# Kernel optimization log

Hardware: AMD Instinct MI355X
Metric: run time of the kernel (lower is better)

Reference implementation:

```python
import jax, jax.numpy as jnp
import numpy as np

LOG_ZERO = -40.0
LOG_EPS = 1e-10

@jax.custom_vjp
def grad_scale(x):
    return x

def _gs_fwd(x):
    return x, None

def _gs_bwd(_, g):
    return (g * 0.01,)

grad_scale.defvjp(_gs_fwd, _gs_bwd)

def to_log_space(x):
    sign_x = jnp.sign(x)
    sign_x = jnp.where(sign_x == 0, jnp.ones_like(sign_x), sign_x)
    abs_x = jnp.abs(x)
    log_x = jnp.where(abs_x > LOG_EPS, jnp.log(jnp.maximum(abs_x, LOG_EPS)), LOG_ZERO)
    return log_x, sign_x

def from_log_space(log_x, sign_x):
    mask = log_x > LOG_ZERO + 1.0
    res = sign_x * jnp.exp(jnp.minimum(grad_scale(log_x), 20.0))
    return jnp.where(mask, res, jnp.zeros_like(res))

def signed_log_add(log_a, sign_a, log_b, sign_b):
    a_is_zero = log_a <= LOG_ZERO + 1.0
    b_is_zero = log_b <= LOG_ZERO + 1.0
    max_log = jnp.maximum(log_a, log_b)
    min_log = jnp.minimum(log_a, log_b)
    diff = min_log - max_log
    a_is_max = log_a >= log_b
    sign_max = jnp.where(a_is_max, sign_a, sign_b)
    sign_min = jnp.where(a_is_max, sign_b, sign_a)
    same_sign = sign_max * sign_min > 0
    exp_diff = jnp.exp(diff)
    log_same = max_log + jnp.log1p(exp_diff)
    log_opp = max_log + jnp.log1p(-jnp.minimum(exp_diff, 0.9999))
    log_result = jnp.where(same_sign, log_same, log_opp)
    sign_result = sign_max
    log_result = jnp.where(a_is_zero, log_b, log_result)
    sign_result = jnp.where(a_is_zero, sign_b, sign_result)
    log_result = jnp.where(b_is_zero & ~a_is_zero, log_a, log_result)
    sign_result = jnp.where(b_is_zero & ~a_is_zero, sign_a, sign_result)
    return log_result, sign_result

def soft_bound_log(log_h):
    return -jax.nn.softplus(-log_h)


def setup_inputs() -> dict:
    key = jax.random.key(0)
    T, B, D = 512, 16, 1024
    k = jax.random.split(key, 4)
    xav = float(np.sqrt(6.0 / (D + D)))  # xavier_uniform bound base
    return {
        'x': jax.random.normal(k[0], (T, B, D), jnp.float32),
        'W_x': jax.random.uniform(k[1], (D, D), jnp.float32, -0.5 * xav, 0.5 * xav),
        'W_alpha': jax.random.uniform(k[2], (D, D), jnp.float32, -0.1 * xav, 0.1 * xav),
        'W_delta': jax.random.uniform(k[3], (D, D), jnp.float32, -0.1 * xav, 0.1 * xav),
        'b': jnp.zeros(D, jnp.float32),
        'b_alpha': jnp.zeros(D, jnp.float32),
        'b_delta': jnp.full((D,), -2.0, jnp.float32),
        'log_r_h': jnp.full((D,), -2.0, jnp.float32),
        'sign_r_h': jnp.ones(D, jnp.float32),
    }


def reference(x, W_x, W_alpha, W_delta, b, b_alpha, b_delta, log_r_h, sign_r_h):
    T, B, D = x.shape
    # Precompute all input projections (the compute-heavy GEMMs) in one shot.
    alpha_raw = jnp.einsum('tbd,ed->tbe', x, W_alpha) + b_alpha        # [T,B,D]
    alpha = 1.0 + jax.nn.softplus(alpha_raw)
    lin = jnp.einsum('tbd,ed->tbe', x, W_x) + b                        # [T,B,D]
    log_input, sign_input = to_log_space(lin)
    delta_raw = jnp.einsum('tbd,ed->tbe', x, W_delta) + b_delta        # [T,B,D]
    log_delta = jax.nn.log_sigmoid(delta_raw)
    log_1m_delta = jax.nn.log_sigmoid(-delta_raw)

    log_h0 = jnp.full((B, D), LOG_ZERO, x.dtype)
    sign_h0 = jnp.ones((B, D), x.dtype)

    def step(carry, inp):
        log_hp, sign_hp = carry
        a_t, log_in, sign_in, log_d, log_1md = inp
        log_rh = log_r_h + log_hp
        sign_rh = sign_r_h * sign_hp
        log_v, sign_v = signed_log_add(log_rh, sign_rh, log_in, sign_in)
        log_cand = soft_bound_log(a_t * log_v)
        log_h_new, sign_h_new = signed_log_add(log_1md + log_hp, sign_hp,
                                               log_d + log_cand, sign_v)
        h_lin = from_log_space(log_h_new, sign_h_new)
        return (log_h_new, sign_h_new), (log_h_new, sign_h_new, h_lin)

    _, (log_hs, sign_hs, h_linear) = jax.lax.scan(
        step, (log_h0, sign_h0), (alpha, log_input, sign_input, log_delta, log_1m_delta))
    log_h = jnp.concatenate([log_h0[None], log_hs], axis=0)    # [T+1,B,D]
    sign_h = jnp.concatenate([sign_h0[None], sign_hs], axis=0) # [T+1,B,D]
    return log_h, sign_h, h_linear
```

## Files before the change

### kernel.cpp

```cpp
#include <hip/hip_runtime.h>
#include <math.h>

#define BD 16384
#define TT 512
#define KDIM 1024
#define NDIM 1024
#define GEMM_M 8192
#define PANEL_Q 320
#define LOGE2F 0.69314718246459960938f

__device__ __forceinline__ float np_expf(float x)   { return expf(x); }
__device__ __forceinline__ float np_logf(float x)   { return logf(x); }
__device__ __forceinline__ float np_log1pf(float x) { return log1pf(x); }

__device__ __forceinline__ float np_softplus(float v) {
    const float e  = np_expf(-fabsf(v));
    const float l1 = np_log1pf(e);
    const float r  = __fadd_rn(fmaxf(v, 0.0f), l1);
    return (v == 0.0f) ? LOGE2F : r;
}

__device__ __forceinline__ void np_sla(float la, float sa, float lb, float sb,
                                       float& lo, float& so) {
    bool az = la <= -39.0f;
    bool bz = lb <= -39.0f;
    float mx = fmaxf(la, lb);
    float mn = fminf(la, lb);
    float diff = __fsub_rn(mn, mx);
    bool amax = la >= lb;
    float smax = amax ? sa : sb;
    float smin = amax ? sb : sa;
    bool same = __fmul_rn(smax, smin) > 0.0f;
    float ed = np_expf(diff);
    float ls  = __fadd_rn(mx, np_log1pf(ed));
    float lop = __fadd_rn(mx, np_log1pf(-fminf(ed, 0.9999f)));
    float l = same ? ls : lop;
    float s = smax;
    l = az ? lb : l;  s = az ? sb : s;
    bool bo = bz && !az;
    l = bo ? la : l;  s = bo ? sa : s;
    lo = l; so = s;
}

__global__ __launch_bounds__(256) void gemm_blas(
    const float* __restrict__ x,
    const float* __restrict__ Wa, const float* __restrict__ Wx, const float* __restrict__ Wd,
    const float* __restrict__ ba, const float* __restrict__ bx, const float* __restrict__ bd,
    float* __restrict__ out_a, float* __restrict__ out_x, float* __restrict__ out_d)
{
    const int z = blockIdx.z;
    const float* W    = (z == 0) ? Wa : (z == 1) ? Wx : Wd;
    const float* bias = (z == 0) ? ba : (z == 1) ? bx : bd;
    float* out        = (z == 0) ? out_a : (z == 1) ? out_x : out_d;

    const int m0 = blockIdx.x * 64;
    const int n0 = blockIdx.y * 64;

    __shared__ float As[16][68];
    __shared__ float Bs[16][68];

    const int tid = threadIdx.x;
    const int lr = tid >> 2;
    const int lc = tid & 3;
    const int ty = tid >> 4;
    const int tx = tid & 15;

    const float* Ap = x + (size_t)(m0 + lr) * KDIM + lc * 4;
    const float* Bp = W + (size_t)(n0 + lr) * KDIM + lc * 4;

    float4 fa = *(const float4*)Ap;
    float4 fb = *(const float4*)Bp;

    float tot[4][4];
    float acc[4][4];
    #pragma unroll
    for (int i = 0; i < 4; ++i)
        #pragma unroll
        for (int j = 0; j < 4; ++j) { tot[i][j] = 0.0f; acc[i][j] = 0.0f; }

    for (int kt = 0; kt < KDIM; kt += 16) {
        if (kt == PANEL_Q || kt == 2 * PANEL_Q || kt == 3 * PANEL_Q) {
            #pragma unroll
            for (int i = 0; i < 4; ++i)
                #pragma unroll
                for (int j = 0; j < 4; ++j) {
                    tot[i][j] = __fadd_rn(tot[i][j], acc[i][j]);
                    acc[i][j] = 0.0f;
                }
        }
        __syncthreads();
        {
            const float* pa = (const float*)&fa;
            const float* pb = (const float*)&fb;
            #pragma unroll
            for (int c = 0; c < 4; ++c) {
                As[lc * 4 + c][lr] = pa[c];
                Bs[lc * 4 + c][lr] = pb[c];
            }
        }
        __syncthreads();
        if (kt + 16 < KDIM) {
            fa = *(const float4*)(Ap + kt + 16);
            fb = *(const float4*)(Bp + kt + 16);
        }
        #pragma unroll
        for (int kk = 0; kk < 16; ++kk) {
            const float4 a = *(const float4*)&As[kk][ty * 4];
            const float4 b = *(const float4*)&Bs[kk][tx * 4];
            const float av[4] = {a.x, a.y, a.z, a.w};
            const float bv[4] = {b.x, b.y, b.z, b.w};
            #pragma unroll
            for (int i = 0; i < 4; ++i)
                #pragma unroll
                for (int j = 0; j < 4; ++j)
                    acc[i][j] = __fmaf_rn(av[i], bv[j], acc[i][j]);
        }
    }
    #pragma unroll
    for (int i = 0; i < 4; ++i)
        #pragma unroll
        for (int j = 0; j < 4; ++j)
            tot[i][j] = __fadd_rn(tot[i][j], acc[i][j]);

    float bj[4];
    #pragma unroll
    for (int j = 0; j < 4; ++j) bj[j] = bias[n0 + tx * 4 + j];

    #pragma unroll
    for (int i = 0; i < 4; ++i) {
        float4 v;
        float* op = out + (size_t)(m0 + ty * 4 + i) * NDIM + n0 + tx * 4;
        v.x = __fadd_rn(tot[i][0], bj[0]);
        v.y = __fadd_rn(tot[i][1], bj[1]);
        v.z = __fadd_rn(tot[i][2], bj[2]);
        v.w = __fadd_rn(tot[i][3], bj[3]);
        *(float4*)op = v;
    }
}

__device__ __forceinline__ void gl_lds(const float* g, float* l) {
    __builtin_amdgcn_global_load_lds(
        (const __attribute__((address_space(1))) void*)g,
        (__attribute__((address_space(3))) void*)l, 4, 0, 0);
}

#define WAITVM(N) do {                                                   \
    asm volatile("s_waitcnt vmcnt(" #N ")" ::: "memory");                \
    __builtin_amdgcn_sched_barrier(0); } while (0)

__global__ __launch_bounds__(192, 1) void scan_kernel(
    float* __restrict__ log_h, float* __restrict__ sign_h, float* __restrict__ h_lin,
    const float* __restrict__ log_r_h, const float* __restrict__ sign_r_h)
{
    __shared__ float Xr[4][5][4][64];
    __shared__ float Or[4][2][4][64];
    __shared__ float Rr[4][12][64];

    const int wv = threadIdx.x >> 6;
    const int ln = threadIdx.x & 63;
    const int idx = blockIdx.x * 64 + ln;

#define ISSUE_LOADS(GG, SL) do {                                         \
    const int _b = (GG) * 4;                                             \
    _Pragma("unroll")                                                    \
    for (int u = 0; u < 4; ++u) {                                        \
        gl_lds(h_lin  + (size_t)(_b + u) * BD + idx,     &Rr[SL][u * 3 + 0][0]); \
        gl_lds(log_h  + (size_t)(_b + u + 1) * BD + idx, &Rr[SL][u * 3 + 1][0]); \
        gl_lds(sign_h + (size_t)(_b + u + 1) * BD + idx, &Rr[SL][u * 3 + 2][0]); \
    } } while (0)

#define XFORM_TO(GG) do {                                                \
    const int _s = (GG) & 3;                                             \
    _Pragma("unroll")                                                    \
    for (int u = 0; u < 4; ++u) {                                        \
        const float araw = Rr[_s][u * 3 + 0][ln];                        \
        const float lin  = Rr[_s][u * 3 + 1][ln];                        \
        const float dr   = Rr[_s][u * 3 + 2][ln];                        \
        Xr[_s][0][u][ln] = __fadd_rn(1.0f, np_softplus(araw));           \
        const float ax = fabsf(lin);                                     \
        Xr[_s][1][u][ln] = (ax > 1e-10f) ? np_logf(fmaxf(ax, 1e-10f))    \
                                         : -40.0f;                       \
        Xr[_s][2][u][ln] = (lin < 0.0f) ? -1.0f : 1.0f;                  \
        const float e  = np_expf(-fabsf(dr));                            \
        const float l1 = np_log1pf(e);                                   \
        const float big = -__fadd_rn(fabsf(dr), l1);                     \
        const float sml = -l1;                                           \
        const float ld0 = (dr > 0.0f) ? sml : big;                       \
        const float lm0 = (dr > 0.0f) ? big : sml;                       \
        Xr[_s][3][u][ln] = (dr == 0.0f) ? -LOGE2F : ld0;                 \
        Xr[_s][4][u][ln] = (dr == 0.0f) ? -LOGE2F : lm0;                 \
    } } while (0)

#define WRITE_GROUP(GG) do {                                             \
    const int _s = (GG) & 3;                                             \
    _Pragma("unroll")                                                    \
    for (int u = 0; u < 4; ++u) {                                        \
        const int t = (GG) * 4 + u;                                      \
        const float lhn = Or[_s][0][u][ln];                              \
        const float shn = Or[_s][1][u][ln];                              \
        const float res = __fmul_rn(shn, np_expf(fminf(lhn, 20.0f)));    \
        const float h = (lhn > -39.0f) ? res : 0.0f;                     \
        log_h[(size_t)(t + 1) * BD + idx] = lhn;                         \
        sign_h[(size_t)(t + 1) * BD + idx] = shn;                        \
        h_lin[(size_t)t * BD + idx] = h;                                 \
    } } while (0)

    float lrh = 0.0f, srh = 0.0f;
    if (wv == 1) {
        const int d = idx & 1023;
        lrh = log_r_h[d];
        srh = sign_r_h[d];
    } else if (wv == 0) {
        ISSUE_LOADS(0, 0);
        ISSUE_LOADS(1, 1);
        WAITVM(0);
        XFORM_TO(0);
        XFORM_TO(1);
        ISSUE_LOADS(2, 2);
    } else {
        log_h[idx] = -40.0f;
        sign_h[idx] = 1.0f;
    }
    __syncthreads();

    float lhp = -40.0f, shp = 1.0f;

    for (int g = 0; g < 128; ++g) {
        if (wv == 0) {
            const int gl = (g + 3 < 128) ? g + 3 : 127;
            ISSUE_LOADS(gl, (g + 3) & 3);
            WAITVM(12);
            if (g + 2 < 128) XFORM_TO(g + 2);
        } else if (wv == 1) {
            const int s = g & 3;
            float xa[4], xli[4], xsi[4], xld[4], xlm[4];
            #pragma unroll
            for (int u = 0; u < 4; ++u) {
                xa[u]  = Xr[s][0][u][ln];
                xli[u] = Xr[s][1][u][ln];
                xsi[u] = Xr[s][2][u][ln];
                xld[u] = Xr[s][3][u][ln];
                xlm[u] = Xr[s][4][u][ln];
            }
            #pragma unroll
            for (int u = 0; u < 4; ++u) {
                const float log_rh  = __fadd_rn(lrh, lhp);
                const float sign_rh = __fmul_rn(srh, shp);
                float lv, sv;
                np_sla(log_rh, sign_rh, xli[u], xsi[u], lv, sv);
                const float tt = __fmul_rn(xa[u], lv);
                const float log_cand = -np_softplus(-tt);
                float lhn, shn;
                np_sla(__fadd_rn(xlm[u], lhp), shp,
                       __fadd_rn(xld[u], log_cand), sv, lhn, shn);
                Or[s][0][u][ln] = lhn;
                Or[s][1][u][ln] = shn;
                lhp = lhn; shp = shn;
            }
        } else {
            if (g > 0) WRITE_GROUP(g - 1);
        }
        __syncthreads();
    }
    if (wv == 2) WRITE_GROUP(127);

#undef ISSUE_LOADS
#undef XFORM_TO
#undef WRITE_GROUP
}

extern "C" void kernel_launch(void* const* d_in, const int* in_sizes, int n_in,
                              void* d_out, int out_size, void* d_ws, size_t ws_size,
                              hipStream_t stream) {
    const float* x        = (const float*)d_in[0];
    const float* W_x      = (const float*)d_in[1];
    const float* W_alpha  = (const float*)d_in[2];
    const float* W_delta  = (const float*)d_in[3];
    const float* b        = (const float*)d_in[4];
    const float* b_alpha  = (const float*)d_in[5];
    const float* b_delta  = (const float*)d_in[6];
    const float* log_r_h  = (const float*)d_in[7];
    const float* sign_r_h = (const float*)d_in[8];

    float* out    = (float*)d_out;
    float* log_h  = out;
    float* sign_h = out + (size_t)513 * BD;
    float* h_lin  = out + (size_t)2 * 513 * BD;

    dim3 ggrid(GEMM_M / 64, NDIM / 64, 3);
    gemm_blas<<<ggrid, dim3(256), 0, stream>>>(
        x, W_alpha, W_x, W_delta, b_alpha, b, b_delta,
        h_lin, log_h + BD, sign_h + BD);

    scan_kernel<<<dim3(BD / 64), dim3(192), 0, stream>>>(
        log_h, sign_h, h_lin, log_r_h, sign_r_h);
}
```

Before: 1.329 ms.

## Fuse GEMM and scan into one persistent kernel with per-slab readiness flags

Merges the three projection GEMMs and the sequential scan into one launch. 256 blocks loop over GEMM tiles in time-slab order and signal per-slab completion counters, while 256 scan blocks spin on those counters so the scan can start before the whole GEMM finishes. The cost targeted is the serialization between the GEMM and the scan. In exchange the GEMM loses its float4 stores and uses agent-scope scalar atomic stores, the scan's async global-to-LDS loads become synchronous atomic loads, and correctness depends on all scan blocks and GEMM blocks being co-resident, otherwise a deadlock is broken only by the spin guard.

```diff
diff --git a/kernel.cpp b/kernel.cpp
--- a/kernel.cpp
+++ b/kernel.cpp
@@ -8,6 +8,9 @@
 #define GEMM_M 8192
 #define PANEL_Q 320
 #define LOGE2F 0.69314718246459960938f
+#define NGEMM 256
+#define NTILE 6144
+#define AGT __HIP_MEMORY_SCOPE_AGENT
 
 __device__ __forceinline__ float np_expf(float x)   { return expf(x); }
 __device__ __forceinline__ float np_logf(float x)   { return logf(x); }
@@ -42,153 +45,154 @@
     lo = l; so = s;
 }
 
-__global__ __launch_bounds__(256) void gemm_blas(
+__device__ __forceinline__ float ld_agent(const float* p) {
+    return __hip_atomic_load(p, __ATOMIC_RELAXED, AGT);
+}
+__device__ __forceinline__ void st_agent(float* p, float v) {
+    __hip_atomic_store(p, v, __ATOMIC_RELAXED, AGT);
+}
+
+__global__ __launch_bounds__(256, 2) void fused(
     const float* __restrict__ x,
     const float* __restrict__ Wa, const float* __restrict__ Wx, const float* __restrict__ Wd,
     const float* __restrict__ ba, const float* __restrict__ bx, const float* __restrict__ bd,
-    float* __restrict__ out_a, float* __restrict__ out_x, float* __restrict__ out_d)
+    const float* __restrict__ log_r_h, const float* __restrict__ sign_r_h,
+    float* __restrict__ log_h, float* __restrict__ sign_h, float* __restrict__ h_lin,
+    int* __restrict__ done)
 {
-    const int z = blockIdx.z;
-    const float* W    = (z == 0) ? Wa : (z == 1) ? Wx : Wd;
-    const float* bias = (z == 0) ? ba : (z == 1) ? bx : bd;
-    float* out        = (z == 0) ? out_a : (z == 1) ? out_x : out_d;
-
-    const int m0 = blockIdx.x * 64;
-    const int n0 = blockIdx.y * 64;
-
-    __shared__ float As[16][68];
-    __shared__ float Bs[16][68];
-
-    const int tid = threadIdx.x;
-    const int lr = tid >> 2;
-    const int lc = tid & 3;
-    const int ty = tid >> 4;
-    const int tx = tid & 15;
-
-    const float* Ap = x + (size_t)(m0 + lr) * KDIM + lc * 4;
-    const float* Bp = W + (size_t)(n0 + lr) * KDIM + lc * 4;
-
-    float4 fa = *(const float4*)Ap;
-    float4 fb = *(const float4*)Bp;
-
-    float tot[4][4];
-    float acc[4][4];
-    #pragma unroll
-    for (int i = 0; i < 4; ++i)
-        #pragma unroll
-        for (int j = 0; j < 4; ++j) { tot[i][j] = 0.0f; acc[i][j] = 0.0f; }
-
-    for (int kt = 0; kt < KDIM; kt += 16) {
-        if (kt == PANEL_Q || kt == 2 * PANEL_Q || kt == 3 * PANEL_Q) {
+    union SMem {
+        struct { float As[16][68]; float Bs[16][68]; } g;
+        struct { float Xr[4][5][4][64]; float Or[4][2][4][64]; } s;
+    };
+    __shared__ SMem sm;
+
+    if (blockIdx.x < NGEMM) {
+        const int tid = threadIdx.x;
+        const int lr = tid >> 2;
+        const int lc = tid & 3;
+        const int ty = tid >> 4;
+        const int tx = tid & 15;
+
+        for (int T = blockIdx.x; T < NTILE; T += NGEMM) {
+            const int m0i = T / 48;
+            const int rem = T % 48;
+            const int z   = rem >> 4;
+            const int n0  = (rem & 15) * 64;
+            const int m0  = m0i * 64;
+            const float* W    = (z == 0) ? Wa : (z == 1) ? Wx : Wd;
+            const float* bias = (z == 0) ? ba : (z == 1) ? bx : bd;
+            float* out = (z == 0) ? h_lin : (z == 1) ? (log_h + BD) : (sign_h + BD);
+
+            const float* Ap = x + (size_t)(m0 + lr) * KDIM + lc * 4;
+            const float* Bp = W + (size_t)(n0 + lr) * KDIM + lc * 4;
+
+            float4 fa = *(const float4*)Ap;
+            float4 fb = *(const float4*)Bp;
+
+            float tot[4][4], acc[4][4];
             #pragma unroll
             for (int i = 0; i < 4; ++i)
                 #pragma unroll
-                for (int j = 0; j < 4; ++j) {
+                for (int j = 0; j < 4; ++j) { tot[i][j] = 0.0f; acc[i][j] = 0.0f; }
+
+            for (int kt = 0; kt < KDIM; kt += 16) {
+                if (kt == PANEL_Q || kt == 2 * PANEL_Q || kt == 3 * PANEL_Q) {
+                    #pragma unroll
+                    for (int i = 0; i < 4; ++i)
+                        #pragma unroll
+                        for (int j = 0; j < 4; ++j) {
+                            tot[i][j] = __fadd_rn(tot[i][j], acc[i][j]);
+                            acc[i][j] = 0.0f;
+                        }
+                }
+                __syncthreads();
+                {
+                    const float* pa = (const float*)&fa;
+                    const float* pb = (const float*)&fb;
+                    #pragma unroll
+                    for (int c = 0; c < 4; ++c) {
+                        sm.g.As[lc * 4 + c][lr] = pa[c];
+                        sm.g.Bs[lc * 4 + c][lr] = pb[c];
+                    }
+                }
+                __syncthreads();
+                if (kt + 16 < KDIM) {
+                    fa = *(const float4*)(Ap + kt + 16);
+                    fb = *(const float4*)(Bp + kt + 16);
+                }
+                #pragma unroll
+                for (int kk = 0; kk < 16; ++kk) {
+                    const float4 a = *(const float4*)&sm.g.As[kk][ty * 4];
+                    const float4 b = *(const float4*)&sm.g.Bs[kk][tx * 4];
+                    const float av[4] = {a.x, a.y, a.z, a.w};
+                    const float bv[4] = {b.x, b.y, b.z, b.w};
+                    #pragma unroll
+                    for (int i = 0; i < 4; ++i)
+                        #pragma unroll
+                        for (int j = 0; j < 4; ++j)
+                            acc[i][j] = __fmaf_rn(av[i], bv[j], acc[i][j]);
+                }
+            }
+            #pragma unroll
+            for (int i = 0; i < 4; ++i)
+                #pragma unroll
+                for (int j = 0; j < 4; ++j)
                     tot[i][j] = __fadd_rn(tot[i][j], acc[i][j]);
-                    acc[i][j] = 0.0f;
-                }
+
+            float bj[4];
+            #pragma unroll
+            for (int j = 0; j < 4; ++j) bj[j] = bias[n0 + tx * 4 + j];
+
+            #pragma unroll
+            for (int i = 0; i < 4; ++i) {
+                float* op = out + (size_t)(m0 + ty * 4 + i) * NDIM + n0 + tx * 4;
+                #pragma unroll
+                for (int j = 0; j < 4; ++j)
+                    st_agent(op + j, __fadd_rn(tot[i][j], bj[j]));
+            }
+            __syncthreads();
+            if (tid == 0)
+                __hip_atomic_fetch_add(&done[m0i], 1, __ATOMIC_RELEASE, AGT);
         }
-        __syncthreads();
-        {
-            const float* pa = (const float*)&fa;
-            const float* pb = (const float*)&fb;
-            #pragma unroll
-            for (int c = 0; c < 4; ++c) {
-                As[lc * 4 + c][lr] = pa[c];
-                Bs[lc * 4 + c][lr] = pb[c];
-            }
-        }
-        __syncthreads();
-        if (kt + 16 < KDIM) {
-            fa = *(const float4*)(Ap + kt + 16);
-            fb = *(const float4*)(Bp + kt + 16);
-        }
-        #pragma unroll
-        for (int kk = 0; kk < 16; ++kk) {
-            const float4 a = *(const float4*)&As[kk][ty * 4];
-            const float4 b = *(const float4*)&Bs[kk][tx * 4];
-            const float av[4] = {a.x, a.y, a.z, a.w};
-            const float bv[4] = {b.x, b.y, b.z, b.w};
-            #pragma unroll
-            for (int i = 0; i < 4; ++i)
-                #pragma unroll
-                for (int j = 0; j < 4; ++j)
-                    acc[i][j] = __fmaf_rn(av[i], bv[j], acc[i][j]);
-        }
-    }
-    #pragma unroll
-    for (int i = 0; i < 4; ++i)
-        #pragma unroll
-        for (int j = 0; j < 4; ++j)
-            tot[i][j] = __fadd_rn(tot[i][j], acc[i][j]);
-
-    float bj[4];
-    #pragma unroll
-    for (int j = 0; j < 4; ++j) bj[j] = bias[n0 + tx * 4 + j];
-
-    #pragma unroll
-    for (int i = 0; i < 4; ++i) {
-        float4 v;
-        float* op = out + (size_t)(m0 + ty * 4 + i) * NDIM + n0 + tx * 4;
-        v.x = __fadd_rn(tot[i][0], bj[0]);
-        v.y = __fadd_rn(tot[i][1], bj[1]);
-        v.z = __fadd_rn(tot[i][2], bj[2]);
-        v.w = __fadd_rn(tot[i][3], bj[3]);
-        *(float4*)op = v;
-    }
-}
-
-__device__ __forceinline__ void gl_lds(const float* g, float* l) {
-    __builtin_amdgcn_global_load_lds(
-        (const __attribute__((address_space(1))) void*)g,
-        (__attribute__((address_space(3))) void*)l, 4, 0, 0);
-}
-
-#define WAITVM(N) do {                                                   \
-    asm volatile("s_waitcnt vmcnt(" #N ")" ::: "memory");                \
-    __builtin_amdgcn_sched_barrier(0); } while (0)
-
-__global__ __launch_bounds__(192, 1) void scan_kernel(
-    float* __restrict__ log_h, float* __restrict__ sign_h, float* __restrict__ h_lin,
-    const float* __restrict__ log_r_h, const float* __restrict__ sign_r_h)
-{
-    __shared__ float Xr[4][5][4][64];
-    __shared__ float Or[4][2][4][64];
-    __shared__ float Rr[4][12][64];
-
-    const int wv = threadIdx.x >> 6;
-    const int ln = threadIdx.x & 63;
-    const int idx = blockIdx.x * 64 + ln;
-
-#define ISSUE_LOADS(GG, SL) do {                                         \
+    } else {
+        const int sb = blockIdx.x - NGEMM;
+        const int wv = threadIdx.x >> 6;
+        const int ln = threadIdx.x & 63;
+        const int idx = sb * 64 + ln;
+
+#define WAIT_SLAB(S) do {                                                \
+    int _guard = 0;                                                      \
+    while (__hip_atomic_load(&done[S], __ATOMIC_ACQUIRE, AGT) < 48) {    \
+        __builtin_amdgcn_s_sleep(2);                                     \
+        if (++_guard > (1 << 27)) break;    \
+    } } while (0)
+
+#define LOAD_XFORM(GG) do {                                              \
+    const int _s = (GG) & 3;                                             \
     const int _b = (GG) * 4;                                             \
+    float ra[4], rl[4], rd[4];                                           \
     _Pragma("unroll")                                                    \
     for (int u = 0; u < 4; ++u) {                                        \
-        gl_lds(h_lin  + (size_t)(_b + u) * BD + idx,     &Rr[SL][u * 3 + 0][0]); \
-        gl_lds(log_h  + (size_t)(_b + u + 1) * BD + idx, &Rr[SL][u * 3 + 1][0]); \
-        gl_lds(sign_h + (size_t)(_b + u + 1) * BD + idx, &Rr[SL][u * 3 + 2][0]); \
-    } } while (0)
-
-#define XFORM_TO(GG) do {                                                \
-    const int _s = (GG) & 3;                                             \
+        ra[u] = ld_agent(h_lin  + (size_t)(_b + u) * BD + idx);          \
+        rl[u] = ld_agent(log_h  + (size_t)(_b + u + 1) * BD + idx);      \
+        rd[u] = ld_agent(sign_h + (size_t)(_b + u + 1) * BD + idx);      \
+    }                                                                    \
     _Pragma("unroll")                                                    \
     for (int u = 0; u < 4; ++u) {                                        \
-        const float araw = Rr[_s][u * 3 + 0][ln];                        \
-        const float lin  = Rr[_s][u * 3 + 1][ln];                        \
-        const float dr   = Rr[_s][u * 3 + 2][ln];                        \
-        Xr[_s][0][u][ln] = __fadd_rn(1.0f, np_softplus(araw));           \
-        const float ax = fabsf(lin);                                     \
-        Xr[_s][1][u][ln] = (ax > 1e-10f) ? np_logf(fmaxf(ax, 1e-10f))    \
-                                         : -40.0f;                       \
-        Xr[_s][2][u][ln] = (lin < 0.0f) ? -1.0f : 1.0f;                  \
+        sm.s.Xr[_s][0][u][ln] = __fadd_rn(1.0f, np_softplus(ra[u]));     \
+        const float ax = fabsf(rl[u]);                                   \
+        sm.s.Xr[_s][1][u][ln] = (ax > 1e-10f) ? np_logf(fmaxf(ax, 1e-10f)) \
+                                              : -40.0f;                  \
+        sm.s.Xr[_s][2][u][ln] = (rl[u] < 0.0f) ? -1.0f : 1.0f;           \
+        const float dr = rd[u];                                          \
         const float e  = np_expf(-fabsf(dr));                            \
         const float l1 = np_log1pf(e);                                   \
         const float big = -__fadd_rn(fabsf(dr), l1);                     \
         const float sml = -l1;                                           \
         const float ld0 = (dr > 0.0f) ? sml : big;                       \
         const float lm0 = (dr > 0.0f) ? big : sml;                       \
-        Xr[_s][3][u][ln] = (dr == 0.0f) ? -LOGE2F : ld0;                 \
-        Xr[_s][4][u][ln] = (dr == 0.0f) ? -LOGE2F : lm0;                 \
+        sm.s.Xr[_s][3][u][ln] = (dr == 0.0f) ? -LOGE2F : ld0;            \
+        sm.s.Xr[_s][4][u][ln] = (dr == 0.0f) ? -LOGE2F : lm0;            \
     } } while (0)
 
 #define WRITE_GROUP(GG) do {                                             \
@@ -196,8 +200,8 @@
     _Pragma("unroll")                                                    \
     for (int u = 0; u < 4; ++u) {                                        \
         const int t = (GG) * 4 + u;                                      \
-        const float lhn = Or[_s][0][u][ln];                              \
-        const float shn = Or[_s][1][u][ln];                              \
+        const float lhn = sm.s.Or[_s][0][u][ln];                         \
+        const float shn = sm.s.Or[_s][1][u][ln];                         \
         const float res = __fmul_rn(shn, np_expf(fminf(lhn, 20.0f)));    \
         const float h = (lhn > -39.0f) ? res : 0.0f;                     \
         log_h[(size_t)(t + 1) * BD + idx] = lhn;                         \
@@ -205,68 +209,67 @@
         h_lin[(size_t)t * BD + idx] = h;                                 \
     } } while (0)
 
-    float lrh = 0.0f, srh = 0.0f;
-    if (wv == 1) {
-        const int d = idx & 1023;
-        lrh = log_r_h[d];
-        srh = sign_r_h[d];
-    } else if (wv == 0) {
-        ISSUE_LOADS(0, 0);
-        ISSUE_LOADS(1, 1);
-        WAITVM(0);
-        XFORM_TO(0);
-        XFORM_TO(1);
-        ISSUE_LOADS(2, 2);
-    } else {
-        log_h[idx] = -40.0f;
-        sign_h[idx] = 1.0f;
-    }
-    __syncthreads();
-
-    float lhp = -40.0f, shp = 1.0f;
-
-    for (int g = 0; g < 128; ++g) {
+        float lrh = 0.0f, srh = 0.0f;
         if (wv == 0) {
-            const int gl = (g + 3 < 128) ? g + 3 : 127;
-            ISSUE_LOADS(gl, (g + 3) & 3);
-            WAITVM(12);
-            if (g + 2 < 128) XFORM_TO(g + 2);
+            WAIT_SLAB(0);
+            LOAD_XFORM(0);
+            WAIT_SLAB(1);
+            LOAD_XFORM(1);
         } else if (wv == 1) {
-            const int s = g & 3;
-            float xa[4], xli[4], xsi[4], xld[4], xlm[4];
-            #pragma unroll
-            for (int u = 0; u < 4; ++u) {
-                xa[u]  = Xr[s][0][u][ln];
-                xli[u] = Xr[s][1][u][ln];
-                xsi[u] = Xr[s][2][u][ln];
-                xld[u] = Xr[s][3][u][ln];
-                xlm[u] = Xr[s][4][u][ln];
-            }
-            #pragma unroll
-            for (int u = 0; u < 4; ++u) {
-                const float log_rh  = __fadd_rn(lrh, lhp);
-                const float sign_rh = __fmul_rn(srh, shp);
-                float lv, sv;
-                np_sla(log_rh, sign_rh, xli[u], xsi[u], lv, sv);
-                const float tt = __fmul_rn(xa[u], lv);
-                const float log_cand = -np_softplus(-tt);
-                float lhn, shn;
-                np_sla(__fadd_rn(xlm[u], lhp), shp,
-                       __fadd_rn(xld[u], log_cand), sv, lhn, shn);
-                Or[s][0][u][ln] = lhn;
-                Or[s][1][u][ln] = shn;
-                lhp = lhn; shp = shn;
-            }
-        } else {
-            if (g > 0) WRITE_GROUP(g - 1);
+            const int d = idx & 1023;
+            lrh = log_r_h[d];
+            srh = sign_r_h[d];
+        } else if (wv == 2) {
+            log_h[idx] = -40.0f;
+            sign_h[idx] = 1.0f;
         }
         __syncthreads();
+
+        float lhp = -40.0f, shp = 1.0f;
+
+        for (int g = 0; g < 128; ++g) {
+            if (wv == 0) {
+                if (g + 2 < 128) {
+                    WAIT_SLAB(g + 2);
+                    LOAD_XFORM(g + 2);
+                }
+            } else if (wv == 1) {
+                const int s = g & 3;
+                float xa[4], xli[4], xsi[4], xld[4], xlm[4];
+                #pragma unroll
+                for (int u = 0; u < 4; ++u) {
+                    xa[u]  = sm.s.Xr[s][0][u][ln];
+                    xli[u] = sm.s.Xr[s][1][u][ln];
+                    xsi[u] = sm.s.Xr[s][2][u][ln];
+                    xld[u] = sm.s.Xr[s][3][u][ln];
+                    xlm[u] = sm.s.Xr[s][4][u][ln];
+                }
+                #pragma unroll
+                for (int u = 0; u < 4; ++u) {
+                    const float log_rh  = __fadd_rn(lrh, lhp);
+                    const float sign_rh = __fmul_rn(srh, shp);
+                    float lv, sv;
+                    np_sla(log_rh, sign_rh, xli[u], xsi[u], lv, sv);
+                    const float tt = __fmul_rn(xa[u], lv);
+                    const float log_cand = -np_softplus(-tt);
+                    float lhn, shn;
+                    np_sla(__fadd_rn(xlm[u], lhp), shp,
+                           __fadd_rn(xld[u], log_cand), sv, lhn, shn);
+                    sm.s.Or[s][0][u][ln] = lhn;
+                    sm.s.Or[s][1][u][ln] = shn;
+                    lhp = lhn; shp = shn;
+                }
+            } else if (wv == 2) {
+                if (g > 0) WRITE_GROUP(g - 1);
+            }
+            __syncthreads();
+        }
+        if (wv == 2) WRITE_GROUP(127);
+
+#undef WAIT_SLAB
+#undef LOAD_XFORM
+#undef WRITE_GROUP
     }
-    if (wv == 2) WRITE_GROUP(127);
-
-#undef ISSUE_LOADS
-#undef XFORM_TO
-#undef WRITE_GROUP
 }
 
 extern "C" void kernel_launch(void* const* d_in, const int* in_sizes, int n_in,
@@ -287,11 +290,10 @@
     float* sign_h = out + (size_t)513 * BD;
     float* h_lin  = out + (size_t)2 * 513 * BD;
 
-    dim3 ggrid(GEMM_M / 64, NDIM / 64, 3);
-    gemm_blas<<<ggrid, dim3(256), 0, stream>>>(
+    int* done = (int*)d_ws;
+    hipMemsetAsync(done, 0, 128 * sizeof(int), stream);
+
+    fused<<<dim3(NGEMM + 256), dim3(256), 0, stream>>>(
         x, W_alpha, W_x, W_delta, b_alpha, b, b_delta,
-        h_lin, log_h + BD, sign_h + BD);
-
-    scan_kernel<<<dim3(BD / 64), dim3(192), 0, stream>>>(
-        log_h, sign_h, h_lin, log_r_h, sign_r_h);
-}
+        log_r_h, sign_r_h, log_h, sign_h, h_lin, done);
+}
```

Result: slower. 3.193 ms (+140.2%).

## Enlarge GEMM block tile to 128x128 with 8x8 per-thread microtile

Applied to the files above, without the earlier changes.

Grows the fp32 GEMM block tile from 64x64 to 128x128, with each thread computing an 8x8 output block instead of 4x4. This raises arithmetic intensity per shared-memory load and halves global traffic per output, aiming to make the SIMT GEMM less bound by LDS and memory bandwidth. The cost is many more registers (128 accumulators plus the partial-sum totals), which lowers occupancy and risks spills, and a grid of only 1536 blocks.

```diff
diff --git a/kernel.cpp b/kernel.cpp
--- a/kernel.cpp
+++ b/kernel.cpp
@@ -53,11 +53,11 @@
     const float* bias = (z == 0) ? ba : (z == 1) ? bx : bd;
     float* out        = (z == 0) ? out_a : (z == 1) ? out_x : out_d;
 
-    const int m0 = blockIdx.x * 64;
-    const int n0 = blockIdx.y * 64;
-
-    __shared__ float As[16][68];
-    __shared__ float Bs[16][68];
+    const int m0 = blockIdx.x * 128;
+    const int n0 = blockIdx.y * 128;
+
+    __shared__ float As[16][132];
+    __shared__ float Bs[16][132];
 
     const int tid = threadIdx.x;
     const int lr = tid >> 2;
@@ -68,73 +68,84 @@
     const float* Ap = x + (size_t)(m0 + lr) * KDIM + lc * 4;
     const float* Bp = W + (size_t)(n0 + lr) * KDIM + lc * 4;
 
-    float4 fa = *(const float4*)Ap;
-    float4 fb = *(const float4*)Bp;
-
-    float tot[4][4];
-    float acc[4][4];
+    float4 aR0 = *(const float4*)(Ap);
+    float4 aR1 = *(const float4*)(Ap + (size_t)64 * KDIM);
+    float4 bR0 = *(const float4*)(Bp);
+    float4 bR1 = *(const float4*)(Bp + (size_t)64 * KDIM);
+
+    float tot[8][8];
+    float acc[8][8];
     #pragma unroll
-    for (int i = 0; i < 4; ++i)
+    for (int i = 0; i < 8; ++i)
         #pragma unroll
-        for (int j = 0; j < 4; ++j) { tot[i][j] = 0.0f; acc[i][j] = 0.0f; }
+        for (int j = 0; j < 8; ++j) { tot[i][j] = 0.0f; acc[i][j] = 0.0f; }
 
     for (int kt = 0; kt < KDIM; kt += 16) {
         if (kt == PANEL_Q || kt == 2 * PANEL_Q || kt == 3 * PANEL_Q) {
             #pragma unroll
-            for (int i = 0; i < 4; ++i)
+            for (int i = 0; i < 8; ++i)
                 #pragma unroll
-                for (int j = 0; j < 4; ++j) {
+                for (int j = 0; j < 8; ++j) {
                     tot[i][j] = __fadd_rn(tot[i][j], acc[i][j]);
                     acc[i][j] = 0.0f;
                 }
         }
         __syncthreads();
         {
-            const float* pa = (const float*)&fa;
-            const float* pb = (const float*)&fb;
+            const float* a0 = (const float*)&aR0;
+            const float* a1 = (const float*)&aR1;
+            const float* b0 = (const float*)&bR0;
+            const float* b1 = (const float*)&bR1;
             #pragma unroll
             for (int c = 0; c < 4; ++c) {
-                As[lc * 4 + c][lr] = pa[c];
-                Bs[lc * 4 + c][lr] = pb[c];
+                As[lc * 4 + c][lr]      = a0[c];
+                As[lc * 4 + c][lr + 64] = a1[c];
+                Bs[lc * 4 + c][lr]      = b0[c];
+                Bs[lc * 4 + c][lr + 64] = b1[c];
             }
         }
         __syncthreads();
         if (kt + 16 < KDIM) {
-            fa = *(const float4*)(Ap + kt + 16);
-            fb = *(const float4*)(Bp + kt + 16);
+            aR0 = *(const float4*)(Ap + kt + 16);
+            aR1 = *(const float4*)(Ap + (size_t)64 * KDIM + kt + 16);
+            bR0 = *(const float4*)(Bp + kt + 16);
+            bR1 = *(const float4*)(Bp + (size_t)64 * KDIM + kt + 16);
         }
         #pragma unroll
         for (int kk = 0; kk < 16; ++kk) {
-            const float4 a = *(const float4*)&As[kk][ty * 4];
-            const float4 b = *(const float4*)&Bs[kk][tx * 4];
-            const float av[4] = {a.x, a.y, a.z, a.w};
-            const float bv[4] = {b.x, b.y, b.z, b.w};
-            #pragma unroll
-            for (int i = 0; i < 4; ++i)
+            const float4 a0 = *(const float4*)&As[kk][ty * 8];
+            const float4 a1 = *(const float4*)&As[kk][ty * 8 + 4];
+            const float4 b0 = *(const float4*)&Bs[kk][tx * 8];
+            const float4 b1 = *(const float4*)&Bs[kk][tx * 8 + 4];
+            const float av[8] = {a0.x, a0.y, a0.z, a0.w, a1.x, a1.y, a1.z, a1.w};
+            const float bv[8] = {b0.x, b0.y, b0.z, b0.w, b1.x, b1.y, b1.z, b1.w};
+            #pragma unroll
+            for (int i = 0; i < 8; ++i)
                 #pragma unroll
-                for (int j = 0; j < 4; ++j)
+                for (int j = 0; j < 8; ++j)
                     acc[i][j] = __fmaf_rn(av[i], bv[j], acc[i][j]);
         }
     }
     #pragma unroll
-    for (int i = 0; i < 4; ++i)
+    for (int i = 0; i < 8; ++i)
         #pragma unroll
-        for (int j = 0; j < 4; ++j)
+        for (int j = 0; j < 8; ++j)
             tot[i][j] = __fadd_rn(tot[i][j], acc[i][j]);
 
-    float bj[4];
+    float bj[8];
     #pragma unroll
-    for (int j = 0; j < 4; ++j) bj[j] = bias[n0 + tx * 4 + j];
+    for (int j = 0; j < 8; ++j) bj[j] = bias[n0 + tx * 8 + j];
 
     #pragma unroll
-    for (int i = 0; i < 4; ++i) {
-        float4 v;
-        float* op = out + (size_t)(m0 + ty * 4 + i) * NDIM + n0 + tx * 4;
-        v.x = __fadd_rn(tot[i][0], bj[0]);
-        v.y = __fadd_rn(tot[i][1], bj[1]);
-        v.z = __fadd_rn(tot[i][2], bj[2]);
-        v.w = __fadd_rn(tot[i][3], bj[3]);
-        *(float4*)op = v;
+    for (int i = 0; i < 8; ++i) {
+        float* op = out + (size_t)(m0 + ty * 8 + i) * NDIM + n0 + tx * 8;
+        float4 v0, v1;
+        v0.x = __fadd_rn(tot[i][0], bj[0]); v0.y = __fadd_rn(tot[i][1], bj[1]);
+        v0.z = __fadd_rn(tot[i][2], bj[2]); v0.w = __fadd_rn(tot[i][3], bj[3]);
+        v1.x = __fadd_rn(tot[i][4], bj[4]); v1.y = __fadd_rn(tot[i][5], bj[5]);
+        v1.z = __fadd_rn(tot[i][6], bj[6]); v1.w = __fadd_rn(tot[i][7], bj[7]);
+        *(float4*)(op)     = v0;
+        *(float4*)(op + 4) = v1;
     }
 }
 
@@ -287,7 +298,7 @@
     float* sign_h = out + (size_t)513 * BD;
     float* h_lin  = out + (size_t)2 * 513 * BD;
 
-    dim3 ggrid(GEMM_M / 64, NDIM / 64, 3);
+    dim3 ggrid(GEMM_M / 128, NDIM / 128, 3);
     gemm_blas<<<ggrid, dim3(256), 0, stream>>>(
         x, W_alpha, W_x, W_delta, b_alpha, b, b_delta,
         h_lin, log_h + BD, sign_h + BD);
```

Result: no change. 1.335 ms (+0.5%).
